# Kernel tuning notes

Measured on AMD Instinct MI355X. Metric: run time of the kernel, lower is better.

Reference implementation:

```python
import jax, jax.numpy as jnp
import numpy as np

LN_EPS = 1e-5

def _ln(x, w, b):
    mu = jnp.mean(x, axis=-1, keepdims=True)
    var = jnp.var(x, axis=-1, keepdims=True)
    return (x - mu) * jax.lax.rsqrt(var + LN_EPS) * w + b

def setup_inputs() -> dict:
    key = jax.random.key(0)
    ks = jax.random.split(key, 16)
    B, T, N = 32, 1024, 77
    D, TD, TE = 512, 256, 2048
    s = lambda fan: 1.0 / np.sqrt(fan)
    return {
        "x": jax.random.normal(ks[0], (B, T, D), jnp.float32),
        "xf": jax.random.normal(ks[1], (B, N, TD), jnp.float32),
        "emb": jax.random.normal(ks[2], (B, TE), jnp.float32),
        "src_mask": jnp.ones((B, T), jnp.float32),
        "cond_type": jax.random.randint(ks[3], (B,), 0, 100, jnp.int64),
        "norm_w": jnp.ones((D,), jnp.float32),
        "norm_b": jnp.zeros((D,), jnp.float32),
        "tnorm_w": jnp.ones((TD,), jnp.float32),
        "tnorm_b": jnp.zeros((TD,), jnp.float32),
        "Wq": jax.random.normal(ks[4], (D, D), jnp.float32) * s(D),
        "bq": jnp.zeros((D,), jnp.float32),
        "Wk": jax.random.normal(ks[5], (D, TD), jnp.float32) * s(TD),
        "bk": jnp.zeros((D,), jnp.float32),
        "Wv": jax.random.normal(ks[6], (D, TD), jnp.float32) * s(TD),
        "bv": jnp.zeros((D,), jnp.float32),
        "emb_w": jax.random.normal(ks[7], (2 * D, TE), jnp.float32) * s(TE),
        "emb_b": jnp.zeros((2 * D,), jnp.float32),
        "snorm_w": jnp.ones((D,), jnp.float32),
        "snorm_b": jnp.zeros((D,), jnp.float32),
        "Wout": jax.random.normal(ks[8], (D, D), jnp.float32) * s(D),
        "bout": jnp.zeros((D,), jnp.float32),
    }

def reference(x, xf, emb, src_mask, cond_type,
              norm_w, norm_b, tnorm_w, tnorm_b,
              Wq, bq, Wk, bk, Wv, bv,
              emb_w, emb_b, snorm_w, snorm_b, Wout, bout):
    B, T, D = x.shape
    N = xf.shape[1]
    H = 8
    dh = D // H
    # projections (no 1/sqrt(dh) scaling, per original)
    q = (_ln(x, norm_w, norm_b) @ Wq.T + bq).reshape(B, T, H, dh)
    xf_n = _ln(xf, tnorm_w, tnorm_b)
    k = (xf_n @ Wk.T + bk).reshape(B, N, H, dh)
    # cond_type gating: text_cond_type = (cond_type % 10 > 0)
    tc = (cond_type % 10 > 0).astype(x.dtype)  # [B]
    bias = (1.0 - tc)[:, None, None, None] * -1000000.0  # [B,1,1,1]
    attn = jnp.einsum('bthd,bnhd->btnh', q, k) + bias
    attn = jax.nn.softmax(attn, axis=2)  # over keys N
    v = (xf_n @ Wv.T + bv) * tc[:, None, None]
    v = v.reshape(B, N, H, dh)
    y = jnp.einsum('btnh,bnhd->bthd', attn, v).reshape(B, T, D)
    # StylizationBlock: silu->linear on emb -> scale/shift, ln, silu->linear, residual
    e = jax.nn.silu(emb) @ emb_w.T + emb_b  # [B, 2D]
    scale, shift = jnp.split(e[:, None, :], 2, axis=2)  # [B,1,D] each
    h = _ln(y, snorm_w, snorm_b) * (1.0 + scale) + shift
    h = jax.nn.silu(h) @ Wout.T + bout
    return x + h
```

## Files before the change

### kernel.cpp

```cpp
#include <hip/hip_runtime.h>
#include <math.h>

#define B_   32
#define T_   1024
#define N_   77
#define D_   512
#define TD_  256
#define TE_  2048
#define H_   8
#define DH_  64

typedef short bf16x8 __attribute__((ext_vector_type(8)));
typedef float f32x4  __attribute__((ext_vector_type(4)));

__device__ __forceinline__ float sigmoidf_fast(float x) {
    return 1.0f / (1.0f + __expf(-x));
}

__device__ __forceinline__ unsigned short f2b(float f) {
    unsigned int u = __float_as_uint(f);
    unsigned int r = u + 0x7FFFu + ((u >> 16) & 1u);
    return (unsigned short)(r >> 16);
}

__device__ __forceinline__ float b2f(short us) {
    return __uint_as_float(((unsigned int)(unsigned short)us) << 16);
}

#define GL16(g, l) __builtin_amdgcn_global_load_lds(                         \
    (const __attribute__((address_space(1))) unsigned int*)(g),              \
    (__attribute__((address_space(3))) unsigned int*)(l), 16, 0, 0)

__global__ __launch_bounds__(256) void ln_xf_kernel(
    const float* __restrict__ x, const float* __restrict__ w, const float* __restrict__ b,
    unsigned short* __restrict__ outb)
{
    int row = blockIdx.x * 4 + (threadIdx.x >> 6);
    int lane = threadIdx.x & 63;
    const float* rp = x + (size_t)row * TD_ + lane * 4;
    float4 v = *(const float4*)rp;
    float s  = v.x + v.y + v.z + v.w;
    float ss = v.x*v.x + v.y*v.y + v.z*v.z + v.w*v.w;
    #pragma unroll
    for (int off = 32; off; off >>= 1) {
        s  += __shfl_xor(s, off);
        ss += __shfl_xor(ss, off);
    }
    float m = s * (1.f / TD_);
    float r = rsqrtf(ss * (1.f / TD_) - m * m + 1e-5f);
    float4 wv = *(const float4*)(w + lane * 4);
    float4 bv = *(const float4*)(b + lane * 4);
    ushort4 o;
    o.x = f2b((v.x - m) * r * wv.x + bv.x);
    o.y = f2b((v.y - m) * r * wv.y + bv.y);
    o.z = f2b((v.z - m) * r * wv.z + bv.z);
    o.w = f2b((v.w - m) * r * wv.w + bv.w);
    *(ushort4*)(outb + (size_t)row * TD_ + lane * 4) = o;
}

__global__ __launch_bounds__(256) void conv_weights_kernel(
    const float* __restrict__ Wq, const float* __restrict__ Wout,
    const float* __restrict__ Wk, const float* __restrict__ Wv,
    unsigned short* __restrict__ wqb, unsigned short* __restrict__ wob,
    unsigned short* __restrict__ wkvb)
{
    int bid = blockIdx.x;
    const float* src; unsigned short* dst;
    if (bid < 128)      { src = Wq;   dst = wqb; }
    else if (bid < 256) { src = Wout; dst = wob;               bid -= 128; }
    else if (bid < 320) { src = Wk;   dst = wkvb;              bid -= 256; }
    else                { src = Wv;   dst = wkvb + D_ * TD_;   bid -= 320; }
    int idx = (bid * 256 + threadIdx.x) * 8;
    float4 v0 = *(const float4*)(src + idx);
    float4 v1 = *(const float4*)(src + idx + 4);
    ushort4 o0 = {f2b(v0.x), f2b(v0.y), f2b(v0.z), f2b(v0.w)};
    ushort4 o1 = {f2b(v1.x), f2b(v1.y), f2b(v1.z), f2b(v1.w)};
    *(ushort4*)(dst + idx)     = o0;
    *(ushort4*)(dst + idx + 4) = o1;
}

__global__ __launch_bounds__(256) void kv_gemm_kernel(
    const unsigned short* __restrict__ Ab,
    const unsigned short* __restrict__ Wb,
    const float* __restrict__ bkp, const float* __restrict__ bvp,
    const int*   __restrict__ cond,
    unsigned short* __restrict__ kout, unsigned short* __restrict__ vout)
{
    constexpr int K = TD_;
    __shared__ __align__(16) unsigned short As[128 * 32];
    __shared__ __align__(16) unsigned short Bs[128 * 32];

    const int tid  = threadIdx.x;
    const int m0   = blockIdx.y * 128;
    const int n0   = blockIdx.x * 128;
    const int lane = tid & 63;
    const int w    = tid >> 6;
    const int l15  = lane & 15;
    const int quad = lane >> 4;
    const int wm   = (w >> 1) * 64;
    const int wn   = (w & 1) * 64;

    const int row_a = tid >> 2;
    const int col16 = tid & 3;

    f32x4 acc[4][4];
    #pragma unroll
    for (int i = 0; i < 4; i++)
        #pragma unroll
        for (int j = 0; j < 4; j++)
            acc[i][j] = (f32x4){0.f, 0.f, 0.f, 0.f};

    const char* gAbase = (const char*)Ab + ((size_t)(m0 + row_a) * K) * 2 + col16 * 16;
    const char* gBbase = (const char*)Wb + ((size_t)(n0 + row_a) * K) * 2 + col16 * 16;
    char* lA = (char*)As + tid * 16;
    char* lB = (char*)Bs + tid * 16;

    for (int k0 = 0; k0 < K; k0 += 32) {
        const char* gA = gAbase + k0 * 2;
        const char* gB = gBbase + k0 * 2;
        GL16(gA, lA);
        GL16(gA + (size_t)64 * K * 2, lA + 4096);
        GL16(gB, lB);
        GL16(gB + (size_t)64 * K * 2, lB + 4096);
        __syncthreads();

        bf16x8 af[4], bfr[4];
        #pragma unroll
        for (int i = 0; i < 4; i++)
            af[i] = *(const bf16x8*)&As[(wm + i * 16 + l15) * 32 + quad * 8];
        #pragma unroll
        for (int j = 0; j < 4; j++)
            bfr[j] = *(const bf16x8*)&Bs[(wn + j * 16 + l15) * 32 + quad * 8];
        #pragma unroll
        for (int i = 0; i < 4; i++)
            #pragma unroll
            for (int j = 0; j < 4; j++)
                acc[i][j] = __builtin_amdgcn_mfma_f32_16x16x32_bf16(af[i], bfr[j], acc[i][j], 0, 0, 0);
        __syncthreads();
    }

    #pragma unroll
    for (int i = 0; i < 4; i++) {
        int mbase = m0 + wm + i * 16 + quad * 4;
        #pragma unroll
        for (int j = 0; j < 4; j++) {
            int n = n0 + wn + j * 16 + l15;
            bool isv = n >= D_;
            int nn = isv ? n - D_ : n;
            float bn = isv ? bvp[nn] : bkp[nn];
            unsigned short* outp = isv ? vout : kout;
            #pragma unroll
            for (int r = 0; r < 4; r++) {
                int m = mbase + r;
                if (m >= B_ * N_) continue;
                float v = acc[i][j][r] + bn;
                if (isv) {
                    int bi = m / N_;
                    v = ((cond[bi] % 10) > 0) ? v : 0.f;
                }
                outp[(size_t)m * D_ + nn] = f2b(v);
            }
        }
    }
}

__global__ __launch_bounds__(256) void emb_gemm_kernel(
    const float* __restrict__ emb, const float* __restrict__ W,
    float* __restrict__ e)
{
    int wid = blockIdx.x * 4 + (threadIdx.x >> 6);
    int lane = threadIdx.x & 63;
    int ngrp = wid >> 3;
    int bgrp = wid & 7;

    float acc[4][4] = {};
    #pragma unroll 2
    for (int it = 0; it < 8; it++) {
        int k = (it * 64 + lane) * 4;
        float4 sv[4], wv[4];
        #pragma unroll
        for (int bi = 0; bi < 4; bi++) {
            float4 t = *(const float4*)&emb[(size_t)(bgrp * 4 + bi) * TE_ + k];
            t.x *= sigmoidf_fast(t.x);
            t.y *= sigmoidf_fast(t.y);
            t.z *= sigmoidf_fast(t.z);
            t.w *= sigmoidf_fast(t.w);
            sv[bi] = t;
        }
        #pragma unroll
        for (int ni = 0; ni < 4; ni++)
            wv[ni] = *(const float4*)&W[(size_t)(ngrp * 4 + ni) * TE_ + k];
        #pragma unroll
        for (int bi = 0; bi < 4; bi++)
            #pragma unroll
            for (int ni = 0; ni < 4; ni++) {
                acc[bi][ni] = fmaf(sv[bi].x, wv[ni].x, acc[bi][ni]);
                acc[bi][ni] = fmaf(sv[bi].y, wv[ni].y, acc[bi][ni]);
                acc[bi][ni] = fmaf(sv[bi].z, wv[ni].z, acc[bi][ni]);
                acc[bi][ni] = fmaf(sv[bi].w, wv[ni].w, acc[bi][ni]);
            }
    }
    #pragma unroll
    for (int bi = 0; bi < 4; bi++)
        #pragma unroll
        for (int ni = 0; ni < 4; ni++) {
            float a = acc[bi][ni];
            #pragma unroll
            for (int off = 32; off; off >>= 1) a += __shfl_xor(a, off);
            if (lane == 0)
                e[(size_t)(bgrp * 4 + bi) * 1024 + ngrp * 4 + ni] = a;
        }
}

__global__ __launch_bounds__(256) void prep_q_kernel(
    const float* __restrict__ x, const float* __restrict__ w, const float* __restrict__ b,
    unsigned short* __restrict__ outb)
{
    int row = blockIdx.x * 4 + (threadIdx.x >> 6);
    int lane = threadIdx.x & 63;
    const float* rp = x + (size_t)row * D_ + lane * 8;
    float4 v0 = *(const float4*)rp;
    float4 v1 = *(const float4*)(rp + 4);
    float s  = v0.x + v0.y + v0.z + v0.w + v1.x + v1.y + v1.z + v1.w;
    float ss = v0.x*v0.x + v0.y*v0.y + v0.z*v0.z + v0.w*v0.w
             + v1.x*v1.x + v1.y*v1.y + v1.z*v1.z + v1.w*v1.w;
    #pragma unroll
    for (int off = 32; off; off >>= 1) {
        s  += __shfl_xor(s, off);
        ss += __shfl_xor(ss, off);
    }
    float m = s * (1.f / D_);
    float r = rsqrtf(ss * (1.f / D_) - m * m + 1e-5f);
    float4 w0 = *(const float4*)(w + lane * 8);
    float4 w1 = *(const float4*)(w + lane * 8 + 4);
    float4 b0 = *(const float4*)(b + lane * 8);
    float4 b1 = *(const float4*)(b + lane * 8 + 4);
    ushort4 o0, o1;
    o0.x = f2b((v0.x - m) * r * w0.x + b0.x);
    o0.y = f2b((v0.y - m) * r * w0.y + b0.y);
    o0.z = f2b((v0.z - m) * r * w0.z + b0.z);
    o0.w = f2b((v0.w - m) * r * w0.w + b0.w);
    o1.x = f2b((v1.x - m) * r * w1.x + b1.x);
    o1.y = f2b((v1.y - m) * r * w1.y + b1.y);
    o1.z = f2b((v1.z - m) * r * w1.z + b1.z);
    o1.w = f2b((v1.w - m) * r * w1.w + b1.w);
    unsigned short* op = outb + (size_t)row * D_ + lane * 8;
    *(ushort4*)op       = o0;
    *(ushort4*)(op + 4) = o1;
}

__global__ __launch_bounds__(256) void prep_h_kernel(
    const unsigned short* __restrict__ y, const float* __restrict__ w, const float* __restrict__ b,
    const float* __restrict__ e, const float* __restrict__ emb_b,
    unsigned short* __restrict__ outb)
{
    int row = blockIdx.x * 4 + (threadIdx.x >> 6);
    int lane = threadIdx.x & 63;
    int bb = row >> 10;
    const unsigned short* rp = y + (size_t)row * D_ + lane * 8;
    bf16x8 yv = *(const bf16x8*)rp;
    float v[8];
    #pragma unroll
    for (int k2 = 0; k2 < 8; k2++) v[k2] = b2f(yv[k2]);
    float s = 0.f, ss = 0.f;
    #pragma unroll
    for (int k2 = 0; k2 < 8; k2++) { s += v[k2]; ss += v[k2] * v[k2]; }
    #pragma unroll
    for (int off = 32; off; off >>= 1) {
        s  += __shfl_xor(s, off);
        ss += __shfl_xor(ss, off);
    }
    float m = s * (1.f / D_);
    float r = rsqrtf(ss * (1.f / D_) - m * m + 1e-5f);
    float4 w0 = *(const float4*)(w + lane * 8);
    float4 w1 = *(const float4*)(w + lane * 8 + 4);
    float4 b0 = *(const float4*)(b + lane * 8);
    float4 b1 = *(const float4*)(b + lane * 8 + 4);
    float wa[8] = {w0.x, w0.y, w0.z, w0.w, w1.x, w1.y, w1.z, w1.w};
    float ba[8] = {b0.x, b0.y, b0.z, b0.w, b1.x, b1.y, b1.z, b1.w};
    const float* ep = e + (size_t)bb * 1024 + lane * 8;
    float4 sc0 = *(const float4*)ep;
    float4 sc1 = *(const float4*)(ep + 4);
    float4 sh0 = *(const float4*)(ep + 512);
    float4 sh1 = *(const float4*)(ep + 512 + 4);
    float4 eb0 = *(const float4*)(emb_b + lane * 8);
    float4 eb1 = *(const float4*)(emb_b + lane * 8 + 4);
    float4 fb0 = *(const float4*)(emb_b + 512 + lane * 8);
    float4 fb1 = *(const float4*)(emb_b + 512 + lane * 8 + 4);
    float sca[8] = {sc0.x + eb0.x, sc0.y + eb0.y, sc0.z + eb0.z, sc0.w + eb0.w,
                    sc1.x + eb1.x, sc1.y + eb1.y, sc1.z + eb1.z, sc1.w + eb1.w};
    float sha[8] = {sh0.x + fb0.x, sh0.y + fb0.y, sh0.z + fb0.z, sh0.w + fb0.w,
                    sh1.x + fb1.x, sh1.y + fb1.y, sh1.z + fb1.z, sh1.w + fb1.w};
    ushort4 o0, o1;
    unsigned short oa[8];
    #pragma unroll
    for (int k2 = 0; k2 < 8; k2++) {
        float hv = ((v[k2] - m) * r * wa[k2] + ba[k2]) * (1.f + sca[k2]) + sha[k2];
        oa[k2] = f2b(hv * sigmoidf_fast(hv));
    }
    o0.x = oa[0]; o0.y = oa[1]; o0.z = oa[2]; o0.w = oa[3];
    o1.x = oa[4]; o1.y = oa[5]; o1.z = oa[6]; o1.w = oa[7];
    unsigned short* op = outb + (size_t)row * D_ + lane * 8;
    *(ushort4*)op       = o0;
    *(ushort4*)(op + 4) = o1;
}

template <int RESID, int OUTBF>
__global__ __launch_bounds__(256) void gemm_bf16_kernel(
    const unsigned short* __restrict__ Ab,
    const unsigned short* __restrict__ Wb,
    const float* __restrict__ bias,
    const float* __restrict__ resid,
    void* __restrict__ Cv)
{
    constexpr int K = 512;
    __shared__ __align__(16) unsigned short As[2][128 * 32];
    __shared__ __align__(16) unsigned short Bs[2][64 * 32];

    const int tid  = threadIdx.x;
    const int m0   = blockIdx.y * 128;
    const int n0   = blockIdx.x * 64;
    const int lane = tid & 63;
    const int w    = tid >> 6;
    const int l15  = lane & 15;
    const int quad = lane >> 4;
    const int wm   = w * 32;

    const int row_s = tid >> 2;
    const int ck    = (tid & 3) ^ (row_s & 3);

    f32x4 acc[2][4];
    #pragma unroll
    for (int i = 0; i < 2; i++)
        #pragma unroll
        for (int j = 0; j < 4; j++)
            acc[i][j] = (f32x4){0.f, 0.f, 0.f, 0.f};

    const char* gA = (const char*)Ab + ((size_t)(m0 + row_s) * K) * 2 + ck * 16;
    const char* gB = (const char*)Wb + ((size_t)(n0 + row_s) * K) * 2 + ck * 16;
    const size_t gA2 = (size_t)64 * K * 2;
    char* lA = (char*)&As[0][0] + tid * 16;
    char* lB = (char*)&Bs[0][0] + tid * 16;

#define STAGE_G(s, buf) do {                                                  \
        const char* pA_ = gA + (s) * 64;                                      \
        GL16(pA_,       lA + (buf) * 8192);                                   \
        GL16(pA_ + gA2, lA + (buf) * 8192 + 4096);                            \
        GL16(gB + (s) * 64, lB + (buf) * 4096);                               \
    } while (0)

    const int sc = (quad ^ (l15 & 3)) << 3;
    bf16x8 af0, af1, bf0, bf1, bf2, bf3;

#define LOADF_G(buf) do {                                                     \
        af0 = *(const bf16x8*)&As[buf][(wm      + l15) * 32 + sc];            \
        af1 = *(const bf16x8*)&As[buf][(wm + 16 + l15) * 32 + sc];            \
        bf0 = *(const bf16x8*)&Bs[buf][(      l15) * 32 + sc];                \
        bf1 = *(const bf16x8*)&Bs[buf][(16 + l15) * 32 + sc];                 \
        bf2 = *(const bf16x8*)&Bs[buf][(32 + l15) * 32 + sc];                 \
        bf3 = *(const bf16x8*)&Bs[buf][(48 + l15) * 32 + sc];                 \
    } while (0)

#define MFMA_G() do {                                                         \
        acc[0][0] = __builtin_amdgcn_mfma_f32_16x16x32_bf16(af0, bf0, acc[0][0], 0, 0, 0); \
        acc[0][1] = __builtin_amdgcn_mfma_f32_16x16x32_bf16(af0, bf1, acc[0][1], 0, 0, 0); \
        acc[0][2] = __builtin_amdgcn_mfma_f32_16x16x32_bf16(af0, bf2, acc[0][2], 0, 0, 0); \
        acc[0][3] = __builtin_amdgcn_mfma_f32_16x16x32_bf16(af0, bf3, acc[0][3], 0, 0, 0); \
        acc[1][0] = __builtin_amdgcn_mfma_f32_16x16x32_bf16(af1, bf0, acc[1][0], 0, 0, 0); \
        acc[1][1] = __builtin_amdgcn_mfma_f32_16x16x32_bf16(af1, bf1, acc[1][1], 0, 0, 0); \
        acc[1][2] = __builtin_amdgcn_mfma_f32_16x16x32_bf16(af1, bf2, acc[1][2], 0, 0, 0); \
        acc[1][3] = __builtin_amdgcn_mfma_f32_16x16x32_bf16(af1, bf3, acc[1][3], 0, 0, 0); \
    } while (0)

    STAGE_G(0, 0);
    __syncthreads();

    #pragma unroll 1
    for (int t = 0; t < 8; t++) {
        LOADF_G(0);
        STAGE_G(2 * t + 1, 1);
        MFMA_G();
        __syncthreads();
        LOADF_G(1);
        if (t < 7) STAGE_G(2 * t + 2, 0);
        MFMA_G();
        __syncthreads();
    }
#undef STAGE_G
#undef LOADF_G
#undef MFMA_G

    float* C = (float*)Cv;
    unsigned short* Cb = (unsigned short*)Cv;
    #pragma unroll
    for (int i = 0; i < 2; i++) {
        int mbase = m0 + wm + i * 16 + quad * 4;
        #pragma unroll
        for (int j = 0; j < 4; j++) {
            int n = n0 + j * 16 + l15;
            float bn = bias[n];
            #pragma unroll
            for (int r = 0; r < 4; r++) {
                size_t off = (size_t)(mbase + r) * 512 + n;
                float v = acc[i][j][r] + bn;
                if (RESID) v += resid[off];
                if (OUTBF) Cb[off] = f2b(v);
                else       C[off]  = v;
            }
        }
    }
}

#define KS2   0
#define VT2   5760
#define PS2   11904
#define SMEM2 18560

__global__ __launch_bounds__(256) void attn_mfma2_kernel(
    const unsigned short* __restrict__ qb,
    const unsigned short* __restrict__ kb,
    const unsigned short* __restrict__ vb,
    unsigned short* __restrict__ yout)
{
    __shared__ __align__(16) unsigned short smem[SMEM2];

    const int tid = threadIdx.x;
    const int t0 = blockIdx.x * 64;
    const int h  = blockIdx.y;
    const int b  = blockIdx.z;

    const int lane = tid & 63;
    const int w    = tid >> 6;
    const int l15  = lane & 15;
    const int quad = lane >> 4;
    const int koff = quad * 8;
    const int mrow = w * 16 + l15;

    const unsigned short* qrow = qb + ((size_t)(b * T_ + t0 + mrow)) * D_ + h * 64 + koff;
    bf16x8 aq0 = *(const bf16x8*)qrow;
    bf16x8 aq1 = *(const bf16x8*)(qrow + 32);

    const unsigned short* kbase = kb + ((size_t)(b * N_)) * D_ + h * 64;
    #pragma unroll
    for (int i = 0; i < 3; i++) {
        int idx = tid + i * 256;
        if (idx < 640) {
            int row = idx >> 3, c8 = idx & 7;
            bf16x8 v = (bf16x8){0, 0, 0, 0, 0, 0, 0, 0};
            if (row < N_) v = *(const bf16x8*)(kbase + (size_t)row * D_ + c8 * 8);
            *(bf16x8*)&smem[KS2 + row * 72 + c8 * 8] = v;
        }
    }
    const unsigned short* vbase = vb + ((size_t)(b * N_)) * D_ + h * 64;
    #pragma unroll
    for (int i = 0; i < 3; i++) {
        int idx = tid + i * 256;
        if (idx < 616) {
            int n = idx >> 3, c8 = idx & 7;
            bf16x8 v = *(const bf16x8*)(vbase + (size_t)n * D_ + c8 * 8);
            int cn = n >> 3, wn = n & 7;
            #pragma unroll
            for (int j = 0; j < 8; j++) {
                int d = c8 * 8 + j;
                int s2 = (j ^ c8) & 3;
                smem[VT2 + d * 96 + ((cn ^ s2) << 3) + wn] = v[j];
            }
        }
    }
    if (tid < 128) {
        int d = tid >> 1, c = 10 + (tid & 1);
        int s2 = (d ^ (d >> 3)) & 3;
        *(bf16x8*)&smem[VT2 + d * 96 + ((c ^ s2) << 3)] = (bf16x8){0, 0, 0, 0, 0, 0, 0, 0};
    }
    {
        int d = tid >> 2, t = tid & 3;
        if (t < 3) {
            int s2 = (d ^ (d >> 3)) & 3;
            smem[VT2 + d * 96 + ((9 ^ s2) << 3) + 5 + t] = 0;
        }
    }
    #pragma unroll
    for (int i = 0; i < 4; i++) {
        int idx = tid + i * 256;
        int row = idx >> 4, col = 80 + (idx & 15);
        smem[PS2 + row * 104 + col] = 0;
    }
    __syncthreads();

    float s[5][4];
    #pragma unroll
    for (int nt = 0; nt < 5; nt++) {
        bf16x8 bk0 = *(const bf16x8*)&smem[KS2 + (nt * 16 + l15) * 72 + koff];
        bf16x8 bk1 = *(const bf16x8*)&smem[KS2 + (nt * 16 + l15) * 72 + 32 + koff];
        f32x4 c = {0.f, 0.f, 0.f, 0.f};
        c = __builtin_amdgcn_mfma_f32_16x16x32_bf16(aq0, bk0, c, 0, 0, 0);
        c = __builtin_amdgcn_mfma_f32_16x16x32_bf16(aq1, bk1, c, 0, 0, 0);
        #pragma unroll
        for (int r = 0; r < 4; r++) s[nt][r] = c[r];
    }
    if (l15 >= N_ - 64) {
        #pragma unroll
        for (int r = 0; r < 4; r++) s[4][r] = -1e30f;
    }
    float li[4];
    #pragma unroll
    for (int r = 0; r < 4; r++) {
        float m = s[0][r];
        #pragma unroll
        for (int nt = 1; nt < 5; nt++) m = fmaxf(m, s[nt][r]);
        m = fmaxf(m, __shfl_xor(m, 1));
        m = fmaxf(m, __shfl_xor(m, 2));
        m = fmaxf(m, __shfl_xor(m, 4));
        m = fmaxf(m, __shfl_xor(m, 8));
        float l = 0.f;
        #pragma unroll
        for (int nt = 0; nt < 5; nt++) {
            float ev = __expf(s[nt][r] - m);
            s[nt][r] = ev;
            l += ev;
        }
        l += __shfl_xor(l, 1);
        l += __shfl_xor(l, 2);
        l += __shfl_xor(l, 4);
        l += __shfl_xor(l, 8);
        li[r] = 1.f / l;
    }
    #pragma unroll
    for (int r = 0; r < 4; r++) {
        int prow = w * 16 + quad * 4 + r;
        #pragma unroll
        for (int nt = 0; nt < 5; nt++) {
            smem[PS2 + prow * 104 + nt * 16 + l15] = f2b(s[nt][r] * li[r]);
        }
    }

    bf16x8 pa0 = *(const bf16x8*)&smem[PS2 + mrow * 104 + 0  + koff];
    bf16x8 pa1 = *(const bf16x8*)&smem[PS2 + mrow * 104 + 32 + koff];
    bf16x8 pa2 = *(const bf16x8*)&smem[PS2 + mrow * 104 + 64 + koff];

    unsigned short* obase = yout + ((size_t)(b * T_ + t0 + w * 16)) * D_ + h * 64;
    #pragma unroll
    for (int dt = 0; dt < 4; dt++) {
        int drow = dt * 16 + l15;
        int s2 = (drow ^ (drow >> 3)) & 3;
        bf16x8 bv0 = *(const bf16x8*)&smem[VT2 + drow * 96 + (((0 + quad) ^ s2) << 3)];
        bf16x8 bv1 = *(const bf16x8*)&smem[VT2 + drow * 96 + (((4 + quad) ^ s2) << 3)];
        bf16x8 bv2 = *(const bf16x8*)&smem[VT2 + drow * 96 + (((8 + quad) ^ s2) << 3)];
        f32x4 c = {0.f, 0.f, 0.f, 0.f};
        c = __builtin_amdgcn_mfma_f32_16x16x32_bf16(pa0, bv0, c, 0, 0, 0);
        c = __builtin_amdgcn_mfma_f32_16x16x32_bf16(pa1, bv1, c, 0, 0, 0);
        c = __builtin_amdgcn_mfma_f32_16x16x32_bf16(pa2, bv2, c, 0, 0, 0);
        #pragma unroll
        for (int r = 0; r < 4; r++) {
            obase[(size_t)(quad * 4 + r) * D_ + dt * 16 + l15] = f2b(c[r]);
        }
    }
}

extern "C" void kernel_launch(void* const* d_in, const int* in_sizes, int n_in,
                              void* d_out, int out_size, void* d_ws, size_t ws_size,
                              hipStream_t stream)
{
    const float* x       = (const float*)d_in[0];
    const float* xf      = (const float*)d_in[1];
    const float* emb     = (const float*)d_in[2];
    const int*   cond    = (const int*)d_in[4];
    const float* norm_w  = (const float*)d_in[5];
    const float* norm_b  = (const float*)d_in[6];
    const float* tnorm_w = (const float*)d_in[7];
    const float* tnorm_b = (const float*)d_in[8];
    const float* Wq      = (const float*)d_in[9];
    const float* bq      = (const float*)d_in[10];
    const float* Wk      = (const float*)d_in[11];
    const float* bk      = (const float*)d_in[12];
    const float* Wv      = (const float*)d_in[13];
    const float* bv      = (const float*)d_in[14];
    const float* emb_w   = (const float*)d_in[15];
    const float* emb_b   = (const float*)d_in[16];
    const float* snorm_w = (const float*)d_in[17];
    const float* snorm_b = (const float*)d_in[18];
    const float* Wout    = (const float*)d_in[19];
    const float* bout    = (const float*)d_in[20];
    float* out = (float*)d_out;

    float* ws = (float*)d_ws;
    float* ebuf = ws;
    unsigned short* u = (unsigned short*)(ebuf + (size_t)B_ * 2 * D_);
    unsigned short* qyb  = u;  u += (size_t)B_ * T_ * D_;
    unsigned short* xfnb = u;  u += (size_t)2560 * TD_;
    unsigned short* kb16 = u;  u += (size_t)B_ * N_ * D_;
    unsigned short* vb16 = u;  u += (size_t)B_ * N_ * D_;
    unsigned short* abh  = u;  u += (size_t)B_ * T_ * D_;
    unsigned short* wqb  = u;  u += (size_t)D_ * D_;
    unsigned short* wob  = u;  u += (size_t)D_ * D_;
    unsigned short* wkvb = u;  u += (size_t)2 * D_ * TD_;
    unsigned short* qb = (unsigned short*)d_out;

    const int BT = B_ * T_;
    const int BN = B_ * N_;

    ln_xf_kernel<<<BN / 4, 256, 0, stream>>>(xf, tnorm_w, tnorm_b, xfnb);
    conv_weights_kernel<<<384, 256, 0, stream>>>(Wq, Wout, Wk, Wv, wqb, wob, wkvb);
    {
        dim3 grid(1024 / 128, 2560 / 128);
        kv_gemm_kernel<<<grid, 256, 0, stream>>>(xfnb, wkvb, bk, bv, cond, kb16, vb16);
    }
    prep_q_kernel<<<BT / 4, 256, 0, stream>>>(x, norm_w, norm_b, abh);
    {
        dim3 grid(D_ / 64, BT / 128);
        gemm_bf16_kernel<0, 1><<<grid, 256, 0, stream>>>(abh, wqb, bq, nullptr, qb);
    }
    emb_gemm_kernel<<<512, 256, 0, stream>>>(emb, emb_w, ebuf);
    {
        dim3 grid(T_ / 64, H_, B_);
        attn_mfma2_kernel<<<grid, 256, 0, stream>>>(qb, kb16, vb16, qyb);
    }
    prep_h_kernel<<<BT / 4, 256, 0, stream>>>(qyb, snorm_w, snorm_b, ebuf, emb_b, abh);
    {
        dim3 grid(D_ / 64, BT / 128);
        gemm_bf16_kernel<1, 0><<<grid, 256, 0, stream>>>(abh, wob, bout, x, out);
    }
}
```

Before: 341.6 us.

## Enlarge GEMM tiles to 128x128, swizzle LDS and remap blocks for XCD locality

The Q and output GEMMs move from 128x64 to 128x128 tiles, with each wave computing a 64x64 sub-tile. This raises MFMA work per LDS load and halves the number of blocks. Both GEMMs, and the KV GEMM, switch to a 1D grid with a block-id swizzle that assigns neighbouring tiles to the same XCD for L2 reuse. The LDS layout gets a new XOR swizzle keyed on row pairs to reduce bank conflicts. In exchange, the larger accumulator raises register use and may lower occupancy, and the grid of 1024 blocks becomes coarser.

```diff
diff --git a/kernel.cpp b/kernel.cpp
--- a/kernel.cpp
+++ b/kernel.cpp
@@ -91,8 +91,10 @@
     __shared__ __align__(16) unsigned short Bs[128 * 32];
 
     const int tid  = threadIdx.x;
-    const int m0   = blockIdx.y * 128;
-    const int n0   = blockIdx.x * 128;
+    int id = blockIdx.x;
+    int swz = (id & 7) * 20 + (id >> 3);
+    const int m0 = (swz >> 3) * 128;
+    const int n0 = (swz & 7) * 128;
     const int lane = tid & 63;
     const int w    = tid >> 6;
     const int l15  = lane & 15;
@@ -101,7 +103,8 @@
     const int wn   = (w & 1) * 64;
 
     const int row_a = tid >> 2;
-    const int col16 = tid & 3;
+    const int ck    = (tid & 3) ^ ((row_a >> 1) & 3);
+    const int sc    = (quad ^ ((l15 >> 1) & 3)) << 3;
 
     f32x4 acc[4][4];
     #pragma unroll
@@ -110,8 +113,8 @@
         for (int j = 0; j < 4; j++)
             acc[i][j] = (f32x4){0.f, 0.f, 0.f, 0.f};
 
-    const char* gAbase = (const char*)Ab + ((size_t)(m0 + row_a) * K) * 2 + col16 * 16;
-    const char* gBbase = (const char*)Wb + ((size_t)(n0 + row_a) * K) * 2 + col16 * 16;
+    const char* gAbase = (const char*)Ab + ((size_t)(m0 + row_a) * K) * 2 + ck * 16;
+    const char* gBbase = (const char*)Wb + ((size_t)(n0 + row_a) * K) * 2 + ck * 16;
     char* lA = (char*)As + tid * 16;
     char* lB = (char*)Bs + tid * 16;
 
@@ -127,10 +130,10 @@
         bf16x8 af[4], bfr[4];
         #pragma unroll
         for (int i = 0; i < 4; i++)
-            af[i] = *(const bf16x8*)&As[(wm + i * 16 + l15) * 32 + quad * 8];
+            af[i] = *(const bf16x8*)&As[(wm + i * 16 + l15) * 32 + sc];
         #pragma unroll
         for (int j = 0; j < 4; j++)
-            bfr[j] = *(const bf16x8*)&Bs[(wn + j * 16 + l15) * 32 + quad * 8];
+            bfr[j] = *(const bf16x8*)&Bs[(wn + j * 16 + l15) * 32 + sc];
         #pragma unroll
         for (int i = 0; i < 4; i++)
             #pragma unroll
@@ -315,61 +318,60 @@
 {
     constexpr int K = 512;
     __shared__ __align__(16) unsigned short As[2][128 * 32];
-    __shared__ __align__(16) unsigned short Bs[2][64 * 32];
+    __shared__ __align__(16) unsigned short Bs[2][128 * 32];
 
     const int tid  = threadIdx.x;
-    const int m0   = blockIdx.y * 128;
-    const int n0   = blockIdx.x * 64;
+    int id = blockIdx.x;
+    int swz = (id & 7) * 128 + (id >> 3);
+    const int m0 = (swz >> 2) * 128;
+    const int n0 = (swz & 3) * 128;
     const int lane = tid & 63;
     const int w    = tid >> 6;
     const int l15  = lane & 15;
     const int quad = lane >> 4;
-    const int wm   = w * 32;
+    const int wm   = (w >> 1) * 64;
+    const int wn   = (w & 1) * 64;
 
     const int row_s = tid >> 2;
-    const int ck    = (tid & 3) ^ (row_s & 3);
-
-    f32x4 acc[2][4];
-    #pragma unroll
-    for (int i = 0; i < 2; i++)
+    const int ck    = (tid & 3) ^ ((row_s >> 1) & 3);
+    const int sc    = (quad ^ ((l15 >> 1) & 3)) << 3;
+
+    f32x4 acc[4][4];
+    #pragma unroll
+    for (int i = 0; i < 4; i++)
         #pragma unroll
         for (int j = 0; j < 4; j++)
             acc[i][j] = (f32x4){0.f, 0.f, 0.f, 0.f};
 
     const char* gA = (const char*)Ab + ((size_t)(m0 + row_s) * K) * 2 + ck * 16;
     const char* gB = (const char*)Wb + ((size_t)(n0 + row_s) * K) * 2 + ck * 16;
-    const size_t gA2 = (size_t)64 * K * 2;
+    const size_t g2 = (size_t)64 * K * 2;
     char* lA = (char*)&As[0][0] + tid * 16;
     char* lB = (char*)&Bs[0][0] + tid * 16;
 
 #define STAGE_G(s, buf) do {                                                  \
-        const char* pA_ = gA + (s) * 64;                                      \
-        GL16(pA_,       lA + (buf) * 8192);                                   \
-        GL16(pA_ + gA2, lA + (buf) * 8192 + 4096);                            \
-        GL16(gB + (s) * 64, lB + (buf) * 4096);                               \
+        GL16(gA + (s) * 64,      lA + (buf) * 8192);                          \
+        GL16(gA + (s) * 64 + g2, lA + (buf) * 8192 + 4096);                   \
+        GL16(gB + (s) * 64,      lB + (buf) * 8192);                          \
+        GL16(gB + (s) * 64 + g2, lB + (buf) * 8192 + 4096);                   \
     } while (0)
 
-    const int sc = (quad ^ (l15 & 3)) << 3;
-    bf16x8 af0, af1, bf0, bf1, bf2, bf3;
-
+    bf16x8 af[4], bfr[4];
 #define LOADF_G(buf) do {                                                     \
-        af0 = *(const bf16x8*)&As[buf][(wm      + l15) * 32 + sc];            \
-        af1 = *(const bf16x8*)&As[buf][(wm + 16 + l15) * 32 + sc];            \
-        bf0 = *(const bf16x8*)&Bs[buf][(      l15) * 32 + sc];                \
-        bf1 = *(const bf16x8*)&Bs[buf][(16 + l15) * 32 + sc];                 \
-        bf2 = *(const bf16x8*)&Bs[buf][(32 + l15) * 32 + sc];                 \
-        bf3 = *(const bf16x8*)&Bs[buf][(48 + l15) * 32 + sc];                 \
+        _Pragma("unroll")                                                     \
+        for (int i = 0; i < 4; i++)                                           \
+            af[i] = *(const bf16x8*)&As[buf][(wm + i * 16 + l15) * 32 + sc];  \
+        _Pragma("unroll")                                                     \
+        for (int j = 0; j < 4; j++)                                           \
+            bfr[j] = *(const bf16x8*)&Bs[buf][(wn + j * 16 + l15) * 32 + sc]; \
     } while (0)
 
 #define MFMA_G() do {                                                         \
-        acc[0][0] = __builtin_amdgcn_mfma_f32_16x16x32_bf16(af0, bf0, acc[0][0], 0, 0, 0); \
-        acc[0][1] = __builtin_amdgcn_mfma_f32_16x16x32_bf16(af0, bf1, acc[0][1], 0, 0, 0); \
-        acc[0][2] = __builtin_amdgcn_mfma_f32_16x16x32_bf16(af0, bf2, acc[0][2], 0, 0, 0); \
-        acc[0][3] = __builtin_amdgcn_mfma_f32_16x16x32_bf16(af0, bf3, acc[0][3], 0, 0, 0); \
-        acc[1][0] = __builtin_amdgcn_mfma_f32_16x16x32_bf16(af1, bf0, acc[1][0], 0, 0, 0); \
-        acc[1][1] = __builtin_amdgcn_mfma_f32_16x16x32_bf16(af1, bf1, acc[1][1], 0, 0, 0); \
-        acc[1][2] = __builtin_amdgcn_mfma_f32_16x16x32_bf16(af1, bf2, acc[1][2], 0, 0, 0); \
-        acc[1][3] = __builtin_amdgcn_mfma_f32_16x16x32_bf16(af1, bf3, acc[1][3], 0, 0, 0); \
+        _Pragma("unroll")                                                     \
+        for (int i = 0; i < 4; i++)                                           \
+            _Pragma("unroll")                                                 \
+            for (int j = 0; j < 4; j++)                                       \
+                acc[i][j] = __builtin_amdgcn_mfma_f32_16x16x32_bf16(af[i], bfr[j], acc[i][j], 0, 0, 0); \
     } while (0)
 
     STAGE_G(0, 0);
@@ -393,11 +395,11 @@
     float* C = (float*)Cv;
     unsigned short* Cb = (unsigned short*)Cv;
     #pragma unroll
-    for (int i = 0; i < 2; i++) {
+    for (int i = 0; i < 4; i++) {
         int mbase = m0 + wm + i * 16 + quad * 4;
         #pragma unroll
         for (int j = 0; j < 4; j++) {
-            int n = n0 + j * 16 + l15;
+            int n = n0 + wn + j * 16 + l15;
             float bn = bias[n];
             #pragma unroll
             for (int r = 0; r < 4; r++) {
@@ -601,23 +603,14 @@
 
     ln_xf_kernel<<<BN / 4, 256, 0, stream>>>(xf, tnorm_w, tnorm_b, xfnb);
     conv_weights_kernel<<<384, 256, 0, stream>>>(Wq, Wout, Wk, Wv, wqb, wob, wkvb);
-    {
-        dim3 grid(1024 / 128, 2560 / 128);
-        kv_gemm_kernel<<<grid, 256, 0, stream>>>(xfnb, wkvb, bk, bv, cond, kb16, vb16);
-    }
+    kv_gemm_kernel<<<160, 256, 0, stream>>>(xfnb, wkvb, bk, bv, cond, kb16, vb16);
     prep_q_kernel<<<BT / 4, 256, 0, stream>>>(x, norm_w, norm_b, abh);
-    {
-        dim3 grid(D_ / 64, BT / 128);
-        gemm_bf16_kernel<0, 1><<<grid, 256, 0, stream>>>(abh, wqb, bq, nullptr, qb);
-    }
+    gemm_bf16_kernel<0, 1><<<1024, 256, 0, stream>>>(abh, wqb, bq, nullptr, qb);
     emb_gemm_kernel<<<512, 256, 0, stream>>>(emb, emb_w, ebuf);
     {
         dim3 grid(T_ / 64, H_, B_);
         attn_mfma2_kernel<<<grid, 256, 0, stream>>>(qb, kb16, vb16, qyb);
     }
     prep_h_kernel<<<BT / 4, 256, 0, stream>>>(qyb, snorm_w, snorm_b, ebuf, emb_b, abh);
-    {
-        dim3 grid(D_ / 64, BT / 128);
-        gemm_bf16_kernel<1, 0><<<grid, 256, 0, stream>>>(abh, wob, bout, x, out);
-    }
-}
+    gemm_bf16_kernel<1, 0><<<1024, 256, 0, stream>>>(abh, wob, bout, x, out);
+}
```

After: 308.4 us. -9.7%, faster.
